# Kernel optimization log

Measured on AMD Instinct MI355X. Metric: run time of the kernel, lower is better.

## Reference

```python
import jax, jax.numpy as jnp
import numpy as np

DIM = 384
HEADS = 8
B, H, W = 2, 128, 128


def _conv(x, w, groups=1):
    # x: [B,C,H,W], w: [Cout, Cin//groups, kh, kw]
    return jax.lax.conv_general_dilated(
        x, w, window_strides=(1, 1), padding='SAME',
        feature_group_count=groups,
        dimension_numbers=('NCHW', 'OIHW', 'NCHW'))


def setup_inputs() -> dict:
    key = jax.random.key(0)
    ks = jax.random.split(key, 12)
    C = DIM
    s = 0.05
    inp = {
        'prompt_feat': jax.random.normal(ks[0], (B, C, H, W), jnp.float32),
        'x_mod': jax.random.normal(ks[1], (B, C, H, W), jnp.float32),
        'y': jax.random.normal(ks[2], (B, C, H, W), jnp.float32),
        'q1_w': jax.random.normal(ks[3], (C, C, 1, 1), jnp.float32) * s,
        'q2_w': jax.random.normal(ks[4], (C, C, 1, 1), jnp.float32) * s,
        'q_dw_w': jax.random.normal(ks[5], (C, 1, 3, 3), jnp.float32) * s,
        'gate_dw_w': jax.random.normal(ks[6], (2 * C, 1, 3, 3), jnp.float32) * s,
        'gate_pw_w': jax.random.normal(ks[7], (C, 2 * C, 1, 1), jnp.float32) * s,
        'kv_w': jax.random.normal(ks[8], (2 * C, C, 1, 1), jnp.float32) * s,
        'kv_dw_w': jax.random.normal(ks[9], (2 * C, 1, 3, 3), jnp.float32) * s,
        'proj_w': jax.random.normal(ks[10], (C, C, 1, 1), jnp.float32) * s,
        'temperature': jnp.ones((HEADS, 1, 1), jnp.float32),
    }
    return inp


def _l2norm(x, eps=1e-12):
    n = jnp.sqrt(jnp.sum(x * x, axis=-1, keepdims=True))
    return x / jnp.maximum(n, eps)


def reference(prompt_feat, x_mod, y, q1_w, q2_w, q_dw_w, gate_dw_w, gate_pw_w,
              kv_w, kv_dw_w, proj_w, temperature):
    b, c, h, w = x_mod.shape
    head = HEADS
    q1 = _conv(prompt_feat, q1_w)              # [B,C,H,W]
    q2 = _conv(x_mod, q2_w)                    # [B,C,H,W]
    cat = jnp.concatenate([q1, q2], axis=1)    # [B,2C,H,W]
    gate = jax.nn.sigmoid(_conv(_conv(cat, gate_dw_w, groups=2 * c), gate_pw_w))
    q = _conv(gate * q1 + (1.0 - gate) * q2, q_dw_w, groups=c)
    kv = _conv(_conv(y, kv_w), kv_dw_w, groups=2 * c)
    k, v = jnp.split(kv, 2, axis=1)            # each [B,C,H,W]
    # rearrange to [B, head, C//head, H*W]
    def to_heads(t):
        return t.reshape(b, head, c // head, h * w)
    q = _l2norm(to_heads(q))
    k = _l2norm(to_heads(k))
    v = to_heads(v)
    # channel attention: [B, head, d, d] with d = C//head
    attn = jnp.einsum('bhcn,bhdn->bhcd', q, k) * temperature[None]
    attn = jax.nn.softmax(attn, axis=-1)
    out = jnp.einsum('bhcd,bhdn->bhcn', attn, v)
    out = out.reshape(b, c, h, w)
    return _conv(out, proj_w)
```

## Files before the change

kernel.cpp:

```cpp
#include <hip/hip_runtime.h>
#include <math.h>

#define HW   16384
#define IMW  128
#define IMH  128
#define CC   384
#define CC2  768
#define NH   8
#define DH   48

typedef unsigned short u16;
typedef __attribute__((ext_vector_type(8))) short short8;
typedef __attribute__((ext_vector_type(16))) float f32x16;

__device__ __forceinline__ void gld16(const u16* g, u16* l) {
    __builtin_amdgcn_global_load_lds(
        (const __attribute__((address_space(1))) unsigned int*)(uintptr_t)g,
        (__attribute__((address_space(3))) unsigned int*)(uintptr_t)l, 16, 0, 0);
}

__device__ __forceinline__ void bf16split(float x, unsigned& hb16, unsigned& lb16) {
    const unsigned u = __float_as_uint(x);
    const unsigned hb = (u + 0x7FFFu + ((u >> 16) & 1u)) & 0xFFFF0000u;
    const float lo = x - __uint_as_float(hb);
    const unsigned v = __float_as_uint(lo);
    hb16 = hb >> 16;
    lb16 = ((v + 0x7FFFu + ((v >> 16) & 1u)) >> 16) & 0xFFFFu;
}

__global__ void wsplit_k(const float* __restrict__ w0, const float* __restrict__ w1,
                         const float* __restrict__ w2, const float* __restrict__ w3,
                         const float* __restrict__ w4,
                         u16* __restrict__ Wh, u16* __restrict__ Wl)
{
    const int i = blockIdx.x * 256 + threadIdx.x;
    if (i >= 1032192) return;
    float x;
    if (i < 147456)      x = w0[i];
    else if (i < 294912) x = w1[i - 147456];
    else if (i < 589824) x = w2[i - 294912];
    else if (i < 884736) x = w3[i - 589824];
    else                 x = w4[i - 884736];
    unsigned h, l;
    bf16split(x, h, l);
    Wh[i] = (u16)h;
    Wl[i] = (u16)l;
}

__global__ __launch_bounds__(256)
void trsplit_k(const float* __restrict__ X, u16* __restrict__ XTh,
               u16* __restrict__ XTl, int C)
{
    __shared__ float tl[64][65];
    const int t  = threadIdx.x;
    const int n0 = blockIdx.x * 64;
    const int k0 = blockIdx.y * 64;
    #pragma unroll
    for (int p = 0; p < 4; ++p) {
        const int kk = p * 16 + (t >> 4);
        const int nn = (t & 15) * 4;
        *(float4*)&tl[kk][nn] = *(const float4*)(X + (size_t)(k0 + kk) * HW + n0 + nn);
    }
    __syncthreads();
    const int n    = t >> 2;
    const int kseg = (t & 3) * 16;
    const int gn   = n0 + n;
    #pragma unroll
    for (int h = 0; h < 2; ++h) {
        unsigned hw_[4], lw_[4];
        #pragma unroll
        for (int i2 = 0; i2 < 4; ++i2) {
            unsigned hp = 0, lp = 0;
            #pragma unroll
            for (int e = 0; e < 2; ++e) {
                unsigned hb, lb;
                bf16split(tl[kseg + h * 8 + i2 * 2 + e][n], hb, lb);
                hp |= hb << (16 * e);
                lp |= lb << (16 * e);
            }
            hw_[i2] = hp; lw_[i2] = lp;
        }
        const int kb   = k0 + kseg + h * 8;
        const int gq   = kb >> 3;
        const int cch  = gq >> 2, qc = gq & 3;
        const int pidx = qc ^ (gn & 3);
        const size_t off = (size_t)gn * C + cch * 32 + pidx * 8;
        *(uint4*)(XTh + off) = make_uint4(hw_[0], hw_[1], hw_[2], hw_[3]);
        *(uint4*)(XTl + off) = make_uint4(lw_[0], lw_[1], lw_[2], lw_[3]);
    }
}

template<int GATE>
__global__ __launch_bounds__(256, 2)
void gemm_mfma_k(const u16* __restrict__ Wh, const u16* __restrict__ Wl,
                 const u16* __restrict__ XTh, const u16* __restrict__ XTl,
                 int K, float* __restrict__ Out,
                 const float* __restrict__ q1p, const float* __restrict__ q2p)
{
    __shared__ u16 Ah[4096], Al[4096], Bh[4096], Bl[4096];
    const int t = threadIdx.x;
    const int w = t >> 6;
    const int l = t & 63;
    const int l31 = l & 31, lh = l >> 5;
    const int nBase = blockIdx.x * 128;
    const int mBase = blockIdx.y * 128;
    const int wm = (w >> 1) * 64, wn = (w & 1) * 64;

    const int jj0 = w * 2, jj1 = jj0 + 1;
    const int offA0 = (mBase + (jj0 & 3) * 32 + (l >> 1)) * K + (jj0 >> 2) * 16 + (l & 1) * 8;
    const int offA1 = (mBase + (jj1 & 3) * 32 + (l >> 1)) * K + (jj1 >> 2) * 16 + (l & 1) * 8;
    const int offB0 = (nBase + jj0 * 16 + (l >> 2)) * K + (l & 3) * 8;
    const int offB1 = (nBase + jj1 * 16 + (l >> 2)) * K + (l & 3) * 8;

    f32x16 acc[2][2];
    #pragma unroll
    for (int i = 0; i < 2; ++i)
        #pragma unroll
        for (int j = 0; j < 2; ++j)
            #pragma unroll
            for (int r = 0; r < 16; ++r) acc[i][j][r] = 0.f;

    const int NC = K >> 5;
    for (int c = 0; c < NC; ++c) {
        const int k0 = c * 32;
        __syncthreads();
        gld16(Wh  + offA0 + k0, Ah + jj0 * 512);
        gld16(Wh  + offA1 + k0, Ah + jj1 * 512);
        gld16(Wl  + offA0 + k0, Al + jj0 * 512);
        gld16(Wl  + offA1 + k0, Al + jj1 * 512);
        gld16(XTh + offB0 + k0, Bh + jj0 * 512);
        gld16(XTh + offB1 + k0, Bh + jj1 * 512);
        gld16(XTl + offB0 + k0, Bl + jj0 * 512);
        gld16(XTl + offB1 + k0, Bl + jj1 * 512);
        __syncthreads();

        short8 ah[2][2], al[2][2], bh[2][2], bl[2][2];
        #pragma unroll
        for (int fm = 0; fm < 2; ++fm)
            #pragma unroll
            for (int ks = 0; ks < 2; ++ks) {
                const int ia = ks * 2048 + (wm + fm * 32 + l31) * 16 + lh * 8;
                ah[fm][ks] = *(const short8*)(Ah + ia);
                al[fm][ks] = *(const short8*)(Al + ia);
            }
        #pragma unroll
        for (int fn = 0; fn < 2; ++fn)
            #pragma unroll
            for (int ks = 0; ks < 2; ++ks) {
                const int nl = wn + fn * 32 + l31;
                const int p  = (ks * 2 + lh) ^ (nl & 3);
                const int ib = nl * 32 + p * 8;
                bh[fn][ks] = *(const short8*)(Bh + ib);
                bl[fn][ks] = *(const short8*)(Bl + ib);
            }
        #pragma unroll
        for (int ks = 0; ks < 2; ++ks)
            #pragma unroll
            for (int fm = 0; fm < 2; ++fm)
                #pragma unroll
                for (int fn = 0; fn < 2; ++fn) {
                    acc[fm][fn] = __builtin_amdgcn_mfma_f32_32x32x16_bf16(ah[fm][ks], bh[fn][ks], acc[fm][fn], 0, 0, 0);
                    acc[fm][fn] = __builtin_amdgcn_mfma_f32_32x32x16_bf16(ah[fm][ks], bl[fn][ks], acc[fm][fn], 0, 0, 0);
                    acc[fm][fn] = __builtin_amdgcn_mfma_f32_32x32x16_bf16(al[fm][ks], bh[fn][ks], acc[fm][fn], 0, 0, 0);
                }
    }

    #pragma unroll
    for (int fm = 0; fm < 2; ++fm)
        #pragma unroll
        for (int fn = 0; fn < 2; ++fn) {
            const int mb = mBase + wm + fm * 32 + lh * 4;
            const int nb = nBase + wn + fn * 32 + l31;
            #pragma unroll
            for (int r = 0; r < 16; ++r) {
                const int m = mb + (r & 3) + 8 * (r >> 2);
                float v = acc[fm][fn][r];
                const size_t off = (size_t)m * HW + nb;
                if (GATE) {
                    const float g = 1.f / (1.f + expf(-v));
                    v = g * q1p[off] + (1.f - g) * q2p[off];
                }
                Out[off] = v;
            }
        }
}

__global__ __launch_bounds__(256)
void dw3x3_k(const float* __restrict__ in, const float* __restrict__ w9,
             float* __restrict__ out)
{
    const int c  = blockIdx.y;
    const int y0 = blockIdx.x * 8;
    __shared__ float tile[10][IMW];

    const float* inc = in + (size_t)c * HW;
    for (int i = threadIdx.x; i < 10 * IMW; i += 256) {
        const int ry = i >> 7, rx = i & 127;
        const int gy = y0 + ry - 1;
        tile[ry][rx] = ((unsigned)gy < (unsigned)IMH) ? inc[gy * IMW + rx] : 0.f;
    }
    float w[9];
    #pragma unroll
    for (int i = 0; i < 9; ++i) w[i] = w9[c * 9 + i];
    __syncthreads();

    const int x  = threadIdx.x & 127;
    const int r0 = threadIdx.x >> 7;
    #pragma unroll
    for (int kk = 0; kk < 4; ++kk) {
        const int ry = r0 * 4 + kk;
        float s = 0.f;
        #pragma unroll
        for (int dy = 0; dy < 3; ++dy) {
            #pragma unroll
            for (int dx = 0; dx < 3; ++dx) {
                const int xx = x + dx - 1;
                const float v = ((unsigned)xx < (unsigned)IMW) ? tile[ry + dy][xx] : 0.f;
                s += w[dy * 3 + dx] * v;
            }
        }
        out[(size_t)c * HW + (y0 + ry) * IMW + x] = s;
    }
}

__global__ __launch_bounds__(256)
void gram_k(const float* __restrict__ q, const float* __restrict__ k,
            float* __restrict__ S, float* __restrict__ ssq, float* __restrict__ ssk)
{
    const int h = blockIdx.y;
    __shared__ float qs[48][65];
    __shared__ float ks[48][65];
    const int t   = threadIdx.x;
    const int tdd = t & 15;
    const int tcc = t >> 4;

    float acc[3][3];
    #pragma unroll
    for (int i = 0; i < 3; ++i)
        #pragma unroll
        for (int j = 0; j < 3; ++j) acc[i][j] = 0.f;
    float sq = 0.f, sk = 0.f;

    for (int ch = 0; ch < 8; ++ch) {
        const int n0 = (blockIdx.x + ch * 32) * 64;
        __syncthreads();
        for (int i = t; i < 48 * 16; i += 256) {
            const int cc = i >> 4, f4 = (i & 15) * 4;
            const float4 qv = *(const float4*)(q + (size_t)(h * 48 + cc) * HW + n0 + f4);
            const float4 kv = *(const float4*)(k + (size_t)(h * 48 + cc) * HW + n0 + f4);
            qs[cc][f4 + 0] = qv.x; qs[cc][f4 + 1] = qv.y; qs[cc][f4 + 2] = qv.z; qs[cc][f4 + 3] = qv.w;
            ks[cc][f4 + 0] = kv.x; ks[cc][f4 + 1] = kv.y; ks[cc][f4 + 2] = kv.z; ks[cc][f4 + 3] = kv.w;
        }
        __syncthreads();
        #pragma unroll 4
        for (int n = 0; n < 64; ++n) {
            float qv[3], kv[3];
            #pragma unroll
            for (int j = 0; j < 3; ++j) { qv[j] = qs[tcc + 16 * j][n]; kv[j] = ks[tdd + 16 * j][n]; }
            #pragma unroll
            for (int i = 0; i < 3; ++i)
                #pragma unroll
                for (int j = 0; j < 3; ++j)
                    acc[i][j] += qv[i] * kv[j];
        }
        if (t < 48) {
            float s = 0.f;
            #pragma unroll 8
            for (int n = 0; n < 64; ++n) s += qs[t][n] * qs[t][n];
            sq += s;
        } else if (t >= 128 && t < 176) {
            const int cc = t - 128;
            float s = 0.f;
            #pragma unroll 8
            for (int n = 0; n < 64; ++n) s += ks[cc][n] * ks[cc][n];
            sk += s;
        }
    }
    #pragma unroll
    for (int i = 0; i < 3; ++i)
        #pragma unroll
        for (int j = 0; j < 3; ++j)
            atomicAdd(&S[(size_t)(h * 48 + tcc + 16 * i) * 48 + tdd + 16 * j], acc[i][j]);
    if (t < 48)                   atomicAdd(&ssq[h * 48 + t], sq);
    else if (t >= 128 && t < 176) atomicAdd(&ssk[h * 48 + t - 128], sk);
}

__global__ void softmax_k(float* __restrict__ S, const float* __restrict__ ssq,
                          const float* __restrict__ ssk, const float* __restrict__ temp)
{
    const int h  = blockIdx.x;
    const int cc = threadIdx.x;
    if (cc >= 48) return;
    const float rq = 1.f / fmaxf(sqrtf(ssq[h * 48 + cc]), 1e-12f);
    const float T  = temp[h];
    float l[48];
    float mx = -1e30f;
    #pragma unroll
    for (int d = 0; d < 48; ++d) {
        const float rk = 1.f / fmaxf(sqrtf(ssk[h * 48 + d]), 1e-12f);
        const float v  = S[(size_t)(h * 48 + cc) * 48 + d] * rq * rk * T;
        l[d] = v;
        mx = fmaxf(mx, v);
    }
    float sum = 0.f;
    #pragma unroll
    for (int d = 0; d < 48; ++d) { const float e = expf(l[d] - mx); l[d] = e; sum += e; }
    const float inv = 1.f / sum;
    #pragma unroll
    for (int d = 0; d < 48; ++d) S[(size_t)(h * 48 + cc) * 48 + d] = l[d] * inv;
}

__global__ __launch_bounds__(256)
void attnv_k(const float* __restrict__ A, const float* __restrict__ v,
             float* __restrict__ out)
{
    const int h  = blockIdx.y;
    const int n0 = blockIdx.x * 64;
    __shared__ float As[48][48];
    __shared__ float Vs[48][64];
    const int t = threadIdx.x;

    for (int i = t; i < 48 * 12; i += 256) {
        const int cc = i / 12, d4 = (i % 12) * 4;
        *(float4*)&As[cc][d4] = *(const float4*)(A + (size_t)(h * 48 + cc) * 48 + d4);
    }
    for (int i = t; i < 48 * 16; i += 256) {
        const int dd = i >> 4, f4 = (i & 15) * 4;
        *(float4*)&Vs[dd][f4] = *(const float4*)(v + (size_t)(h * 48 + dd) * HW + n0 + f4);
    }
    __syncthreads();

    const int n4 = (t & 15) * 4;
    const int cg = t >> 4;
    float o[3][4];
    #pragma unroll
    for (int i = 0; i < 3; ++i)
        #pragma unroll
        for (int j = 0; j < 4; ++j) o[i][j] = 0.f;

    #pragma unroll
    for (int d0 = 0; d0 < 48; d0 += 8) {
        float vr[8][4];
        #pragma unroll
        for (int di = 0; di < 8; ++di) {
            const float4 x = *(const float4*)&Vs[d0 + di][n4];
            vr[di][0] = x.x; vr[di][1] = x.y; vr[di][2] = x.z; vr[di][3] = x.w;
        }
        #pragma unroll
        for (int ci = 0; ci < 3; ++ci) {
            const int cc = cg * 3 + ci;
            const float4 a0 = *(const float4*)&As[cc][d0];
            const float4 a1 = *(const float4*)&As[cc][d0 + 4];
            const float a[8] = {a0.x, a0.y, a0.z, a0.w, a1.x, a1.y, a1.z, a1.w};
            #pragma unroll
            for (int di = 0; di < 8; ++di)
                #pragma unroll
                for (int j = 0; j < 4; ++j)
                    o[ci][j] += a[di] * vr[di][j];
        }
    }
    #pragma unroll
    for (int ci = 0; ci < 3; ++ci) {
        const int cc = cg * 3 + ci;
        *(float4*)(out + (size_t)(h * 48 + cc) * HW + n0 + n4) =
            make_float4(o[ci][0], o[ci][1], o[ci][2], o[ci][3]);
    }
}

extern "C" void kernel_launch(void* const* d_in, const int* in_sizes, int n_in,
                              void* d_out, int out_size, void* d_ws, size_t ws_size,
                              hipStream_t stream)
{
    const float* prompt    = (const float*)d_in[0];
    const float* xmod      = (const float*)d_in[1];
    const float* yin       = (const float*)d_in[2];
    const float* q1_w      = (const float*)d_in[3];
    const float* q2_w      = (const float*)d_in[4];
    const float* q_dw_w    = (const float*)d_in[5];
    const float* gate_dw_w = (const float*)d_in[6];
    const float* gate_pw_w = (const float*)d_in[7];
    const float* kv_w      = (const float*)d_in[8];
    const float* kv_dw_w   = (const float*)d_in[9];
    const float* proj_w    = (const float*)d_in[10];
    const float* temp      = (const float*)d_in[11];
    float* out = (float*)d_out;
    float* ws  = (float*)d_ws;

    const size_t BUF  = (size_t)CC2 * HW;
    const size_t HALF = (size_t)CC * HW;
    float* q12 = ws;
    float* t1  = ws + BUF;
    float* t2  = ws + 2 * BUF;
    u16*   Wh  = (u16*)(ws + 3 * BUF);
    u16*   Wl  = Wh + 1032192;
    float* S   = ws + 3 * BUF + 1032192;
    float* ssq = S + NH * DH * DH;
    float* ssk = ssq + CC;

    const int WO_Q1 = 0, WO_Q2 = 147456, WO_GATE = 294912, WO_KV = 589824, WO_PROJ = 884736;

    u16* XT2h = (u16*)t2;
    u16* XT2l = XT2h + (size_t)HW * CC2;
    u16* XT1h = (u16*)t1;
    u16* XT1l = XT1h + (size_t)HW * CC;

    const dim3 blk(256);

    wsplit_k<<<dim3(4032), blk, 0, stream>>>(q1_w, q2_w, gate_pw_w, kv_w, proj_w, Wh, Wl);

    for (int b = 0; b < 2; ++b) {
        const size_t ib = (size_t)b * CC * HW;

        trsplit_k<<<dim3(256, 6), blk, 0, stream>>>(prompt + ib, XT1h, XT1l, CC);
        gemm_mfma_k<0><<<dim3(128, 3), blk, 0, stream>>>(Wh + WO_Q1, Wl + WO_Q1, XT1h, XT1l, CC, q12, nullptr, nullptr);
        trsplit_k<<<dim3(256, 6), blk, 0, stream>>>(xmod + ib, XT1h, XT1l, CC);
        gemm_mfma_k<0><<<dim3(128, 3), blk, 0, stream>>>(Wh + WO_Q2, Wl + WO_Q2, XT1h, XT1l, CC, q12 + HALF, nullptr, nullptr);
        dw3x3_k<<<dim3(16, CC2), blk, 0, stream>>>(q12, gate_dw_w, t1);
        trsplit_k<<<dim3(256, 12), blk, 0, stream>>>(t1, XT2h, XT2l, CC2);
        gemm_mfma_k<1><<<dim3(128, 3), blk, 0, stream>>>(Wh + WO_GATE, Wl + WO_GATE, XT2h, XT2l, CC2, q12, q12, q12 + HALF);
        dw3x3_k<<<dim3(16, CC), blk, 0, stream>>>(q12, q_dw_w, q12 + HALF);
        trsplit_k<<<dim3(256, 6), blk, 0, stream>>>(yin + ib, XT1h, XT1l, CC);
        gemm_mfma_k<0><<<dim3(128, 6), blk, 0, stream>>>(Wh + WO_KV, Wl + WO_KV, XT1h, XT1l, CC, t2, nullptr, nullptr);
        dw3x3_k<<<dim3(16, CC2), blk, 0, stream>>>(t2, kv_dw_w, t1);
        hipMemsetAsync(S, 0, (NH * DH * DH + 2 * CC) * sizeof(float), stream);
        gram_k<<<dim3(32, NH), blk, 0, stream>>>(q12 + HALF, t1, S, ssq, ssk);
        softmax_k<<<dim3(NH), dim3(64), 0, stream>>>(S, ssq, ssk, temp);
        attnv_k<<<dim3(HW / 64, NH), blk, 0, stream>>>(S, t1 + HALF, t2);
        trsplit_k<<<dim3(256, 6), blk, 0, stream>>>(t2, XT1h, XT1l, CC);
        gemm_mfma_k<0><<<dim3(128, 3), blk, 0, stream>>>(Wh + WO_PROJ, Wl + WO_PROJ, XT1h, XT1l, CC, out + ib, nullptr, nullptr);
    }
}
```

Baseline: 813.2 us.

## Double-buffer GEMM LDS tiles and switch to fragment-ordered LDS layout

The MFMA GEMM now keeps two LDS buffers and issues the global-to-LDS loads for chunk c+1 before computing chunk c, with one barrier per iteration instead of two. This is meant to overlap global-memory latency with the MFMA work. The B-operand global layout drops its XOR swizzle, and both A and B tiles are staged so each lane reads its fragment at a contiguous l*8 offset, removing the swizzle index math. LDS use doubles to 64 KB per block, which may limit occupancy at launch_bounds(256,2). The single barrier at the end of each iteration must be correctly placed to avoid races with the async loads.

```diff
diff --git a/kernel.cpp b/kernel.cpp
--- a/kernel.cpp
+++ b/kernel.cpp
@@ -80,11 +80,8 @@
             }
             hw_[i2] = hp; lw_[i2] = lp;
         }
-        const int kb   = k0 + kseg + h * 8;
-        const int gq   = kb >> 3;
-        const int cch  = gq >> 2, qc = gq & 3;
-        const int pidx = qc ^ (gn & 3);
-        const size_t off = (size_t)gn * C + cch * 32 + pidx * 8;
+        const int kb = k0 + kseg + h * 8;
+        const size_t off = (size_t)gn * C + kb;
         *(uint4*)(XTh + off) = make_uint4(hw_[0], hw_[1], hw_[2], hw_[3]);
         *(uint4*)(XTl + off) = make_uint4(lw_[0], lw_[1], lw_[2], lw_[3]);
     }
@@ -97,20 +94,34 @@
                  int K, float* __restrict__ Out,
                  const float* __restrict__ q1p, const float* __restrict__ q2p)
 {
-    __shared__ u16 Ah[4096], Al[4096], Bh[4096], Bl[4096];
+    __shared__ u16 Ah[2][4096], Al[2][4096], Bh[2][4096], Bl[2][4096];
     const int t = threadIdx.x;
     const int w = t >> 6;
     const int l = t & 63;
     const int l31 = l & 31, lh = l >> 5;
     const int nBase = blockIdx.x * 128;
     const int mBase = blockIdx.y * 128;
-    const int wm = (w >> 1) * 64, wn = (w & 1) * 64;
+    const int wmh = (w >> 1) * 2;
+    const int wnh = (w & 1) * 2;
 
     const int jj0 = w * 2, jj1 = jj0 + 1;
-    const int offA0 = (mBase + (jj0 & 3) * 32 + (l >> 1)) * K + (jj0 >> 2) * 16 + (l & 1) * 8;
-    const int offA1 = (mBase + (jj1 & 3) * 32 + (l >> 1)) * K + (jj1 >> 2) * 16 + (l & 1) * 8;
-    const int offB0 = (nBase + jj0 * 16 + (l >> 2)) * K + (l & 3) * 8;
-    const int offB1 = (nBase + jj1 * 16 + (l >> 2)) * K + (l & 3) * 8;
+    const int offA0 = (mBase + (jj0 & 3) * 32 + l31) * K + (jj0 >> 2) * 16 + lh * 8;
+    const int offA1 = (mBase + (jj1 & 3) * 32 + l31) * K + (jj1 >> 2) * 16 + lh * 8;
+    const int offB0 = (nBase + (jj0 & 3) * 32 + l31) * K + (jj0 >> 2) * 16 + lh * 8;
+    const int offB1 = (nBase + (jj1 & 3) * 32 + l31) * K + (jj1 >> 2) * 16 + lh * 8;
+    const int ldst0 = jj0 * 512, ldst1 = jj1 * 512;
+
+#define STAGE(buf, k0)                                  \
+    do {                                                \
+        gld16(Wh  + offA0 + (k0), Ah[buf] + ldst0);     \
+        gld16(Wh  + offA1 + (k0), Ah[buf] + ldst1);     \
+        gld16(Wl  + offA0 + (k0), Al[buf] + ldst0);     \
+        gld16(Wl  + offA1 + (k0), Al[buf] + ldst1);     \
+        gld16(XTh + offB0 + (k0), Bh[buf] + ldst0);     \
+        gld16(XTh + offB1 + (k0), Bh[buf] + ldst1);     \
+        gld16(XTl + offB0 + (k0), Bl[buf] + ldst0);     \
+        gld16(XTl + offB1 + (k0), Bl[buf] + ldst1);     \
+    } while (0)
 
     f32x16 acc[2][2];
     #pragma unroll
@@ -121,37 +132,28 @@
             for (int r = 0; r < 16; ++r) acc[i][j][r] = 0.f;
 
     const int NC = K >> 5;
+    STAGE(0, 0);
+    __syncthreads();
+    int p = 0;
     for (int c = 0; c < NC; ++c) {
-        const int k0 = c * 32;
-        __syncthreads();
-        gld16(Wh  + offA0 + k0, Ah + jj0 * 512);
-        gld16(Wh  + offA1 + k0, Ah + jj1 * 512);
-        gld16(Wl  + offA0 + k0, Al + jj0 * 512);
-        gld16(Wl  + offA1 + k0, Al + jj1 * 512);
-        gld16(XTh + offB0 + k0, Bh + jj0 * 512);
-        gld16(XTh + offB1 + k0, Bh + jj1 * 512);
-        gld16(XTl + offB0 + k0, Bl + jj0 * 512);
-        gld16(XTl + offB1 + k0, Bl + jj1 * 512);
-        __syncthreads();
+        if (c + 1 < NC) STAGE(p ^ 1, (c + 1) * 32);
 
         short8 ah[2][2], al[2][2], bh[2][2], bl[2][2];
         #pragma unroll
-        for (int fm = 0; fm < 2; ++fm)
-            #pragma unroll
-            for (int ks = 0; ks < 2; ++ks) {
-                const int ia = ks * 2048 + (wm + fm * 32 + l31) * 16 + lh * 8;
-                ah[fm][ks] = *(const short8*)(Ah + ia);
-                al[fm][ks] = *(const short8*)(Al + ia);
+        for (int ks = 0; ks < 2; ++ks)
+            #pragma unroll
+            for (int fm = 0; fm < 2; ++fm) {
+                const int ia = (ks * 4 + wmh + fm) * 512 + l * 8;
+                ah[fm][ks] = *(const short8*)(&Ah[p][ia]);
+                al[fm][ks] = *(const short8*)(&Al[p][ia]);
             }
         #pragma unroll
-        for (int fn = 0; fn < 2; ++fn)
-            #pragma unroll
-            for (int ks = 0; ks < 2; ++ks) {
-                const int nl = wn + fn * 32 + l31;
-                const int p  = (ks * 2 + lh) ^ (nl & 3);
-                const int ib = nl * 32 + p * 8;
-                bh[fn][ks] = *(const short8*)(Bh + ib);
-                bl[fn][ks] = *(const short8*)(Bl + ib);
+        for (int ks = 0; ks < 2; ++ks)
+            #pragma unroll
+            for (int fn = 0; fn < 2; ++fn) {
+                const int ib = (ks * 4 + wnh + fn) * 512 + l * 8;
+                bh[fn][ks] = *(const short8*)(&Bh[p][ib]);
+                bl[fn][ks] = *(const short8*)(&Bl[p][ib]);
             }
         #pragma unroll
         for (int ks = 0; ks < 2; ++ks)
@@ -163,14 +165,17 @@
                     acc[fm][fn] = __builtin_amdgcn_mfma_f32_32x32x16_bf16(ah[fm][ks], bl[fn][ks], acc[fm][fn], 0, 0, 0);
                     acc[fm][fn] = __builtin_amdgcn_mfma_f32_32x32x16_bf16(al[fm][ks], bh[fn][ks], acc[fm][fn], 0, 0, 0);
                 }
-    }
+        __syncthreads();
+        p ^= 1;
+    }
+#undef STAGE
 
     #pragma unroll
     for (int fm = 0; fm < 2; ++fm)
         #pragma unroll
         for (int fn = 0; fn < 2; ++fn) {
-            const int mb = mBase + wm + fm * 32 + lh * 4;
-            const int nb = nBase + wn + fn * 32 + l31;
+            const int mb = mBase + (wmh + fm) * 32 + lh * 4;
+            const int nb = nBase + (wnh + fn) * 32 + l31;
             #pragma unroll
             for (int r = 0; r < 16; ++r) {
                 const int m = mb + (r & 3) + 8 * (r >> 2);
```

Measured after the change: 889.9 us. 1.09x slower.
